# Optimization experiments

Hardware: AMD Instinct MI355X
Metric: run time of the kernel (lower is better)

## Reference

```python
import math
import jax, jax.numpy as jnp
import numpy as np

EMBED_DIM = 1024
N_HEADS = 16
HEAD_DIM = EMBED_DIM // N_HEADS
B, T = 4, 2048


def setup_inputs() -> dict:
    key = jax.random.key(0)
    k1, k2, k3 = jax.random.split(key, 3)
    scale_in = 1.0 / math.sqrt(EMBED_DIM)
    return {
        "x": jax.random.normal(k1, (B, T, EMBED_DIM), dtype=jnp.float32),
        "direction": 0,  # 0=FORWARD (causal), 1=RETRODICTION (anti-causal), 2=CORRECTION (causal)
        "qkv_w": jax.random.normal(k2, (EMBED_DIM, 3 * EMBED_DIM), dtype=jnp.float32) * scale_in,
        "qkv_b": jnp.zeros((3 * EMBED_DIM,), dtype=jnp.float32),
        "proj_w": jax.random.normal(k3, (EMBED_DIM, EMBED_DIM), dtype=jnp.float32) * scale_in,
        "proj_b": jnp.zeros((EMBED_DIM,), dtype=jnp.float32),
    }


def reference(x, direction, qkv_w, qkv_b, proj_w, proj_b):
    Bx, Tx, C = x.shape
    qkv = x @ qkv_w + qkv_b                        # [B,T,3C]
    q, k, v = jnp.split(qkv, 3, axis=-1)
    # [B,T,C] -> [B,H,T,D]
    def heads(t):
        return t.reshape(Bx, Tx, N_HEADS, HEAD_DIM).transpose(0, 2, 1, 3)
    q, k, v = heads(q), heads(k), heads(v)
    scale = 1.0 / math.sqrt(HEAD_DIM)
    attn = jnp.einsum('bhqd,bhkd->bhqk', q, k) * scale
    rows = jnp.arange(Tx)[:, None]
    cols = jnp.arange(Tx)[None, :]
    if direction == 1:  # RETRODICTION -> anti-causal (upper triangular allowed)
        mask = cols >= rows
    else:               # FORWARD / CORRECTION -> causal
        mask = cols <= rows
    attn = jnp.where(mask[None, None], attn, -jnp.inf)
    attn = jax.nn.softmax(attn, axis=-1)  # dropout p=0 -> identity
    out = jnp.einsum('bhqk,bhkd->bhqd', attn, v)   # [B,H,T,D]
    out = out.transpose(0, 2, 1, 3).reshape(Bx, Tx, C)
    return out @ proj_w + proj_b
```

## Files before the change

### kernel.cpp

```cpp
#include <hip/hip_runtime.h>
#include <math.h>

typedef __bf16 bf16_t;
typedef bf16_t bf16x8 __attribute__((ext_vector_type(8)));
typedef bf16_t bf16x4 __attribute__((ext_vector_type(4)));
typedef float  f32x4  __attribute__((ext_vector_type(4)));
typedef float  floatv4 __attribute__((ext_vector_type(4)));

#define AS1 __attribute__((address_space(1)))
#define AS3 __attribute__((address_space(3)))

static __device__ __forceinline__ void gld_lds16(const void* g, void* l) {
  __builtin_amdgcn_global_load_lds((const AS1 unsigned int*)g,
                                   (AS3 unsigned int*)l, 16, 0, 0);
}
static __device__ __forceinline__ void block_sync() {
  asm volatile("" ::: "memory");
  __builtin_amdgcn_s_barrier();
  asm volatile("" ::: "memory");
}

__global__ __launch_bounds__(256) void k_cast(const float* __restrict__ in,
                                              bf16_t* __restrict__ out, int n4) {
  int i = blockIdx.x * 256 + threadIdx.x;
  if (i >= n4) return;
  floatv4 v = ((const floatv4*)in)[i];
  bf16x4 o;
  o.x = (bf16_t)v.x; o.y = (bf16_t)v.y; o.z = (bf16_t)v.z; o.w = (bf16_t)v.w;
  ((bf16x4*)out)[i] = o;
}

__global__ __launch_bounds__(256) void k_transpose_cast(const float* __restrict__ in,
                                                        bf16_t* __restrict__ out,
                                                        int R, int Cc) {
  __shared__ float tile[32][33];
  int c0 = blockIdx.x * 32, r0 = blockIdx.y * 32;
  int tx = threadIdx.x, ty = threadIdx.y;
#pragma unroll
  for (int i = 0; i < 32; i += 8)
    tile[ty + i][tx] = in[(size_t)(r0 + ty + i) * Cc + c0 + tx];
  __syncthreads();
#pragma unroll
  for (int i = 0; i < 32; i += 8)
    out[(size_t)(c0 + ty + i) * R + r0 + tx] = (bf16_t)tile[tx][ty + i];
}


__global__ __launch_bounds__(512, 2) void k_gemm_qkv(
    const bf16_t* __restrict__ A, const bf16_t* __restrict__ Bt,
    const float* __restrict__ bias,
    bf16_t* __restrict__ qo, bf16_t* __restrict__ ko, bf16_t* __restrict__ vto) {
  const int K = 1024;
  __shared__ __align__(16) char smem[147456];
  const int m0 = blockIdx.x * 256, n0 = blockIdx.y * 128;
  const int t = threadIdx.x, lane = t & 63, wv = t >> 6;
  const int ln15 = lane & 15, lhi = lane >> 4;
  const int wr = wv >> 1, wc = wv & 1;

  f32x4 acc[4][4];
#pragma unroll
  for (int m = 0; m < 4; ++m)
#pragma unroll
    for (int n = 0; n < 4; ++n) acc[m][n] = (f32x4){0.f, 0.f, 0.f, 0.f};

  const bf16_t* aSrc = A + (size_t)(m0 + (t >> 7) * 16 + ln15) * K + ((t >> 6) & 1) * 32 + lhi * 8;
  const bf16_t* bSrc = Bt + (size_t)(n0 + (t >> 7) * 16 + ln15) * K + ((t >> 6) & 1) * 32 + lhi * 8;
  const int dstOff = t * 16;

  auto stage = [&](int k0, char* base) {
#pragma unroll
    for (int c = 0; c < 4; ++c)
      gld_lds16(aSrc + (size_t)c * 64 * K + k0, base + c * 8192 + dstOff);
#pragma unroll
    for (int c = 0; c < 2; ++c)
      gld_lds16(bSrc + (size_t)c * 64 * K + k0, base + 32768 + c * 8192 + dstOff);
  };
  auto compute = [&](const char* base) {
    const bf16_t* Ab = (const bf16_t*)base;
    const bf16_t* Bb = (const bf16_t*)(base + 32768);
#pragma unroll
    for (int kk = 0; kk < 2; ++kk) {
      bf16x8 af[4], bf[4];
#pragma unroll
      for (int m = 0; m < 4; ++m)
        af[m] = *(const bf16x8*)(Ab + ((wr * 4 + m) * 2 + kk) * 512 + lane * 8);
#pragma unroll
      for (int n = 0; n < 4; ++n)
        bf[n] = *(const bf16x8*)(Bb + ((wc * 4 + n) * 2 + kk) * 512 + lane * 8);
      __builtin_amdgcn_s_setprio(1);
#pragma unroll
      for (int m = 0; m < 4; ++m)
#pragma unroll
        for (int n = 0; n < 4; ++n)
          acc[m][n] = __builtin_amdgcn_mfma_f32_16x16x32_bf16(af[m], bf[n], acc[m][n], 0, 0, 0);
      __builtin_amdgcn_s_setprio(0);
    }
  };

  char* pc = smem;
  char* p1 = smem + 49152;
  char* p2 = smem + 98304;
  stage(0, pc);
  stage(64, p1);
#pragma unroll 1
  for (int it = 0; it < 16; ++it) {
    if (it + 2 < 16) {
      stage((it + 2) * 64, p2);
      asm volatile("s_waitcnt vmcnt(12)" ::: "memory");
    } else if (it + 1 < 16) {
      asm volatile("s_waitcnt vmcnt(6)" ::: "memory");
    } else {
      asm volatile("s_waitcnt vmcnt(0)" ::: "memory");
    }
    block_sync();
    compute(pc);
    block_sync();
    char* old = pc; pc = p1; p1 = p2; p2 = old;
  }

  const int which = n0 >> 10;
  const float bscale = (which == 0) ? 0.18033688011112042f : 1.0f;
  bf16_t* L = (bf16_t*)smem;
#pragma unroll
  for (int n = 0; n < 4; ++n) {
    const int col = wc * 64 + n * 16 + ln15;
    const float bv = bias[n0 + col];
#pragma unroll
    for (int m = 0; m < 4; ++m)
#pragma unroll
      for (int j = 0; j < 4; ++j) {
        const int row = wr * 64 + m * 16 + lhi * 4 + j;
        const bf16_t ob = (bf16_t)((acc[m][n][j] + bv) * bscale);
        if (which == 2) L[col * 264 + row] = ob;
        else            L[row * 132 + col] = ob;
      }
  }
  block_sync();
  const int bq = m0 >> 11, ttb = m0 & 2047;
  if (which == 2) {
#pragma unroll
    for (int c = 0; c < 8; ++c) {
      const int idx = c * 512 + t;
      const int vcol = idx >> 5, r8 = (idx & 31) * 8;
      bf16x8 v8 = *(const bf16x8*)&L[vcol * 264 + r8];
      const int cc = (n0 + vcol) & 1023;
      const int hh = cc >> 6, d = cc & 63;
      *(bf16x8*)&vto[((size_t)(bq * 16 + hh) * 64 + d) * 2048 + ttb + r8] = v8;
    }
  } else {
    bf16_t* dst = (which == 0) ? qo : ko;
#pragma unroll
    for (int c = 0; c < 8; ++c) {
      const int idx = c * 512 + t;
      const int row = idx >> 4, c8 = (idx & 15) * 8;
      bf16x8 v8 = *(const bf16x8*)&L[row * 132 + c8];
      const int cc = (n0 & 1023) + c8;
      const int hh = cc >> 6, d = cc & 63;
      *(bf16x8*)&dst[((size_t)(bq * 16 + hh) * 2048 + ttb + row) * 64 + d] = v8;
    }
  }
}

__global__ __launch_bounds__(256) void k_attn3(
    const bf16_t* __restrict__ q, const bf16_t* __restrict__ k,
    const bf16_t* __restrict__ vt, const int* __restrict__ dirp,
    bf16_t* __restrict__ a2) {
  const int T = 2048;
  __shared__ __align__(16) bf16_t smem[16384];
  const int bh = blockIdx.x, b = bh >> 4, h = bh & 15;
  const int jb = blockIdx.y;
  const int t = threadIdx.x, lane = t & 63, w = t >> 6;
  const int ln15 = lane & 15, lhi = lane >> 4;
  const bool anti = (*dirp == 1);

  const bf16_t* kbase = k + (size_t)bh * T * 64;
  const bf16_t* vbase = vt + (size_t)bh * 64 * T;

  auto stage = [&](int kc0, int buf) {
    char* Kd = (char*)smem + buf * 16384;
    char* Vd = Kd + 8192;
#pragma unroll
    for (int s = 0; s < 2; ++s) {
      const int qk = s * 4 + (t >> 6);
      const int krow = kc0 + (qk >> 2) * 32 + ((qk >> 1) & 1) * 4 +
                       ((lane & 15) >> 2) * 8 + (lane & 3);
      const int kcolb = (lane >> 4) * 16 + (qk & 1) * 64;
      gld_lds16((const char*)kbase + (size_t)krow * 128 + kcolb,
                Kd + s * 4096 + t * 16);
      const int gv = qk;
      const int vd = (gv & 3) * 16 + (lane & 15);
      gld_lds16((const char*)vbase + (size_t)vd * 4096 + (size_t)kc0 * 2 +
                    (gv >> 2) * 64 + (lane >> 4) * 16,
                Vd + s * 4096 + t * 16);
    }
  };

#pragma unroll 1
  for (int sel = 0; sel < 2; ++sel) {
    const int qt = sel ? (31 - jb) : jb;
    const int q0 = qt * 64 + w * 16;
    const int qrow = q0 + ln15;

    const bf16_t* qp = q + ((size_t)bh * T + qrow) * 64 + lhi * 8;
    bf16x8 qf0 = *(const bf16x8*)qp;
    bf16x8 qf1 = *(const bf16x8*)(qp + 32);

    f32x4 acc[4];
#pragma unroll
    for (int g = 0; g < 4; ++g) acc[g] = (f32x4){0.f, 0.f, 0.f, 0.f};
    float mrun = -3.0e38f, lrun = 0.f;

    const int kt0 = anti ? qt : 0;
    const int nb = anti ? (32 - qt) : (qt + 1);

    stage(kt0 * 64, 0);
#pragma unroll 1
    for (int i = 0; i < nb; ++i) {
      const int kt = kt0 + i;
      const int buf = i & 1;
      if (i + 1 < nb) {
        stage((kt + 1) * 64, buf ^ 1);
        asm volatile("s_waitcnt vmcnt(4)" ::: "memory");
      } else {
        asm volatile("s_waitcnt vmcnt(0)" ::: "memory");
      }
      block_sync();
      const bf16_t* Kb = smem + buf * 8192;
      const bf16_t* Vb = Kb + 4096;

      float sc[16];
#pragma unroll
      for (int kh = 0; kh < 2; ++kh) {
        bf16x8 k0 = *(const bf16x8*)(Kb + (kh * 4 + 0) * 512 + lane * 8);
        bf16x8 k1 = *(const bf16x8*)(Kb + (kh * 4 + 1) * 512 + lane * 8);
        bf16x8 k2 = *(const bf16x8*)(Kb + (kh * 4 + 2) * 512 + lane * 8);
        bf16x8 k3 = *(const bf16x8*)(Kb + (kh * 4 + 3) * 512 + lane * 8);
        const f32x4 zz = (f32x4){0.f, 0.f, 0.f, 0.f};
        f32x4 slo = __builtin_amdgcn_mfma_f32_16x16x32_bf16(k0, qf0, zz, 0, 0, 0);
        slo = __builtin_amdgcn_mfma_f32_16x16x32_bf16(k1, qf1, slo, 0, 0, 0);
        f32x4 shi = __builtin_amdgcn_mfma_f32_16x16x32_bf16(k2, qf0, zz, 0, 0, 0);
        shi = __builtin_amdgcn_mfma_f32_16x16x32_bf16(k3, qf1, shi, 0, 0, 0);
#pragma unroll
        for (int j = 0; j < 4; ++j) {
          sc[kh * 8 + j] = slo[j];
          sc[kh * 8 + 4 + j] = shi[j];
        }
      }
      if (kt == qt) {
#pragma unroll
        for (int e = 0; e < 16; ++e) {
          const int col = kt * 64 + (e >> 3) * 32 + lhi * 8 + (e & 7);
          const bool ok = anti ? (col >= qrow) : (col <= qrow);
          sc[e] = ok ? sc[e] : -3.0e38f;
        }
      }
      float lmax = sc[0];
#pragma unroll
      for (int e = 1; e < 16; ++e) lmax = fmaxf(lmax, sc[e]);
      if (!__all(lmax <= mrun + 8.f)) {
        float vm = lmax;
        vm = fmaxf(vm, __shfl_xor(vm, 16));
        vm = fmaxf(vm, __shfl_xor(vm, 32));
        const float mn = fmaxf(mrun, vm);
        const float al = __builtin_amdgcn_exp2f(mrun - mn);
        lrun *= al;
#pragma unroll
        for (int g = 0; g < 4; ++g) acc[g] *= al;
        mrun = mn;
      }
      bf16x8 pb0, pb1;
      float rs = 0.f;
#pragma unroll
      for (int e = 0; e < 8; ++e) {
        float p = __builtin_amdgcn_exp2f(sc[e] - mrun);
        rs += p; pb0[e] = (bf16_t)p;
      }
#pragma unroll
      for (int e = 0; e < 8; ++e) {
        float p = __builtin_amdgcn_exp2f(sc[8 + e] - mrun);
        rs += p; pb1[e] = (bf16_t)p;
      }
      lrun += rs;
#pragma unroll
      for (int dg = 0; dg < 4; ++dg) {
        bf16x8 v0 = *(const bf16x8*)(Vb + dg * 512 + lane * 8);
        acc[dg] = __builtin_amdgcn_mfma_f32_16x16x32_bf16(v0, pb0, acc[dg], 0, 0, 0);
      }
#pragma unroll
      for (int dg = 0; dg < 4; ++dg) {
        bf16x8 v1 = *(const bf16x8*)(Vb + (4 + dg) * 512 + lane * 8);
        acc[dg] = __builtin_amdgcn_mfma_f32_16x16x32_bf16(v1, pb1, acc[dg], 0, 0, 0);
      }
      block_sync();
    }

    lrun += __shfl_xor(lrun, 16);
    lrun += __shfl_xor(lrun, 32);
    const float inv = __builtin_amdgcn_rcpf(lrun);
    bf16_t* op = a2 + ((size_t)b * T + qrow) * 1024 + h * 64 + lhi * 4;
#pragma unroll
    for (int g = 0; g < 4; ++g) {
      bf16x4 o4;
#pragma unroll
      for (int jx = 0; jx < 4; ++jx) o4[jx] = (bf16_t)(acc[g][jx] * inv);
      *(bf16x4*)(op + g * 16) = o4;
    }
  }
}

__global__ __launch_bounds__(512, 2) void k_gemm_proj(
    const bf16_t* __restrict__ A, const bf16_t* __restrict__ Bt,
    const float* __restrict__ bias, float* __restrict__ out) {
  const int K = 1024;
  __shared__ __align__(16) char smem[147456];
  const int m0 = blockIdx.x * 256, n0 = blockIdx.y * 128;
  const int t = threadIdx.x, lane = t & 63, wv = t >> 6;
  const int ln15 = lane & 15, lhi = lane >> 4;
  const int wr = wv >> 1, wc = wv & 1;

  f32x4 acc[4][4];
#pragma unroll
  for (int m = 0; m < 4; ++m)
#pragma unroll
    for (int n = 0; n < 4; ++n) acc[m][n] = (f32x4){0.f, 0.f, 0.f, 0.f};

  const bf16_t* aSrc = A + (size_t)(m0 + (t >> 7) * 16 + ln15) * K + ((t >> 6) & 1) * 32 + lhi * 8;
  const bf16_t* bSrc = Bt + (size_t)(n0 + (t >> 7) * 16 + ln15) * K + ((t >> 6) & 1) * 32 + lhi * 8;
  const int dstOff = t * 16;

  auto stage = [&](int k0, char* base) {
#pragma unroll
    for (int c = 0; c < 4; ++c)
      gld_lds16(aSrc + (size_t)c * 64 * K + k0, base + c * 8192 + dstOff);
#pragma unroll
    for (int c = 0; c < 2; ++c)
      gld_lds16(bSrc + (size_t)c * 64 * K + k0, base + 32768 + c * 8192 + dstOff);
  };
  auto compute = [&](const char* base) {
    const bf16_t* Ab = (const bf16_t*)base;
    const bf16_t* Bb = (const bf16_t*)(base + 32768);
#pragma unroll
    for (int kk = 0; kk < 2; ++kk) {
      bf16x8 af[4], bf[4];
#pragma unroll
      for (int m = 0; m < 4; ++m)
        af[m] = *(const bf16x8*)(Ab + ((wr * 4 + m) * 2 + kk) * 512 + lane * 8);
#pragma unroll
      for (int n = 0; n < 4; ++n)
        bf[n] = *(const bf16x8*)(Bb + ((wc * 4 + n) * 2 + kk) * 512 + lane * 8);
      __builtin_amdgcn_s_setprio(1);
#pragma unroll
      for (int m = 0; m < 4; ++m)
#pragma unroll
        for (int n = 0; n < 4; ++n)
          acc[m][n] = __builtin_amdgcn_mfma_f32_16x16x32_bf16(af[m], bf[n], acc[m][n], 0, 0, 0);
      __builtin_amdgcn_s_setprio(0);
    }
  };

  char* pc = smem;
  char* p1 = smem + 49152;
  char* p2 = smem + 98304;
  stage(0, pc);
  stage(64, p1);
#pragma unroll 1
  for (int it = 0; it < 16; ++it) {
    if (it + 2 < 16) {
      stage((it + 2) * 64, p2);
      asm volatile("s_waitcnt vmcnt(12)" ::: "memory");
    } else if (it + 1 < 16) {
      asm volatile("s_waitcnt vmcnt(6)" ::: "memory");
    } else {
      asm volatile("s_waitcnt vmcnt(0)" ::: "memory");
    }
    block_sync();
    compute(pc);
    block_sync();
    char* old = pc; pc = p1; p1 = p2; p2 = old;
  }

#pragma unroll
  for (int n = 0; n < 4; ++n) {
    const int col = n0 + wc * 64 + n * 16 + ln15;
    const float bv = bias[col];
#pragma unroll
    for (int m = 0; m < 4; ++m)
#pragma unroll
      for (int j = 0; j < 4; ++j) {
        const int row = m0 + wr * 64 + m * 16 + lhi * 4 + j;
        out[(size_t)row * 1024 + col] = acc[m][n][j] + bv;
      }
  }
}

extern "C" void kernel_launch(void* const* d_in, const int* in_sizes, int n_in,
                              void* d_out, int out_size, void* d_ws, size_t ws_size,
                              hipStream_t stream) {
  (void)in_sizes; (void)n_in; (void)out_size; (void)ws_size;
  const float* x      = (const float*)d_in[0];
  const int*   dirp   = (const int*)d_in[1];
  const float* qkv_w  = (const float*)d_in[2];
  const float* qkv_b  = (const float*)d_in[3];
  const float* proj_w = (const float*)d_in[4];
  const float* proj_b = (const float*)d_in[5];
  float* out = (float*)d_out;

  char* ws = (char*)d_ws;
  bf16_t* xb   = (bf16_t*)(ws);
  bf16_t* wq_t = (bf16_t*)(ws + 16777216);
  bf16_t* wp_t = (bf16_t*)(ws + 23068672);
  bf16_t* qb   = (bf16_t*)(ws + 25165824);
  bf16_t* kb   = (bf16_t*)(ws + 41943040);
  bf16_t* vtb  = (bf16_t*)(ws + 58720256);
  bf16_t* a2   = xb;

  k_cast<<<8192, 256, 0, stream>>>(x, xb, 2097152);
  k_transpose_cast<<<dim3(96, 32), dim3(32, 8), 0, stream>>>(qkv_w, wq_t, 1024, 3072);
  k_transpose_cast<<<dim3(32, 32), dim3(32, 8), 0, stream>>>(proj_w, wp_t, 1024, 1024);
  k_gemm_qkv<<<dim3(32, 24), 512, 0, stream>>>(xb, wq_t, qkv_b, qb, kb, vtb);
  k_attn3<<<dim3(64, 16), 256, 0, stream>>>(qb, kb, vtb, dirp, a2);
  k_gemm_proj<<<dim3(32, 8), 512, 0, stream>>>(a2, wp_t, proj_b, out);
}
```

Measured before the change: 204.5 us.

## Enlarge QKV GEMM tile to 256x256 with interleaved LDS-load/MFMA schedule

The QKV projection GEMM now computes 256x256 output tiles per block (8x4 MFMA fragments per wave) instead of 256x128, halving the grid to 32x12. The main loop is double buffered instead of triple buffered, and each K-step is split into four phases that interleave LDS fragment reads, global-to-LDS staging and MFMA groups with explicit waits and barriers. The epilogue writes the wider tile in two halves through LDS. This aims to raise arithmetic intensity and overlap memory with compute, at the cost of more accumulator registers, many more barriers per iteration, and fewer blocks (384) to fill the CUs.

```diff
diff --git a/kernel.cpp b/kernel.cpp
--- a/kernel.cpp
+++ b/kernel.cpp
@@ -45,11 +45,291 @@
     out[(size_t)(c0 + ty + i) * R + r0 + tx] = (bf16_t)tile[tx][ty + i];
 }
 
-
 __global__ __launch_bounds__(512, 2) void k_gemm_qkv(
     const bf16_t* __restrict__ A, const bf16_t* __restrict__ Bt,
     const float* __restrict__ bias,
     bf16_t* __restrict__ qo, bf16_t* __restrict__ ko, bf16_t* __restrict__ vto) {
+  const int K = 1024;
+  __shared__ __align__(16) char smem[131072];
+  const int m0 = blockIdx.x * 256, n0 = blockIdx.y * 256;
+  const int t = threadIdx.x, lane = t & 63, wv = t >> 6;
+  const int ln15 = lane & 15, lhi = lane >> 4;
+  const int wr = wv >> 2, wc = wv & 3;
+
+  f32x4 acc[8][4];
+#pragma unroll
+  for (int m = 0; m < 8; ++m)
+#pragma unroll
+    for (int n = 0; n < 4; ++n) acc[m][n] = (f32x4){0.f, 0.f, 0.f, 0.f};
+  bf16x8 af[4], bfr[4];
+
+  auto stageA = [&](int r, int k0, char* buf) {
+    const int s = r * 8 + wv;
+    gld_lds16(A + (size_t)(m0 + (s & 15) * 16 + ln15) * K + k0 + (s >> 4) * 32 + lhi * 8,
+              buf + r * 8192 + t * 16);
+  };
+  auto stageB = [&](int r, int k0, char* buf) {
+    const int s = r * 8 + wv;
+    gld_lds16(Bt + (size_t)(n0 + (s & 15) * 16 + ln15) * K + k0 + (s >> 4) * 32 + lhi * 8,
+              buf + 32768 + r * 8192 + t * 16);
+  };
+
+#define LDA(kk, mb) do { _Pragma("unroll") for (int m = 0; m < 4; ++m) \
+    af[m] = *(const bf16x8*)((const bf16_t*)bufC + ((kk) * 16 + wr * 8 + (mb) + m) * 512 + lane * 8); } while (0)
+#define LDB(kk) do { _Pragma("unroll") for (int n = 0; n < 4; ++n) \
+    bfr[n] = *(const bf16x8*)((const bf16_t*)(bufC + 32768) + ((kk) * 16 + wc * 4 + n) * 512 + lane * 8); } while (0)
+#define MFMA16(mb) do { __builtin_amdgcn_s_setprio(1); _Pragma("unroll") \
+    for (int m = 0; m < 4; ++m) { _Pragma("unroll") for (int n = 0; n < 4; ++n) \
+      acc[(mb) + m][n] = __builtin_amdgcn_mfma_f32_16x16x32_bf16(af[m], bfr[n], acc[(mb) + m][n], 0, 0, 0); } \
+    __builtin_amdgcn_s_setprio(0); } while (0)
+#define WAIT_LGK() do { asm volatile("s_waitcnt lgkmcnt(0)" ::: "memory"); \
+    __builtin_amdgcn_sched_barrier(0); } while (0)
+
+  char* bufC = smem;
+  char* bufN = smem + 65536;
+  stageA(0, 0, bufC); stageA(1, 0, bufC); stageB(0, 0, bufC); stageB(1, 0, bufC);
+  stageA(2, 0, bufC); stageA(3, 0, bufC); stageB(2, 0, bufC); stageB(3, 0, bufC);
+  asm volatile("s_waitcnt vmcnt(4)" ::: "memory");
+  block_sync();
+
+#pragma unroll 1
+  for (int it = 0; it < 16; ++it) {
+    const int k0n = (it + 1) * 64;
+    const bool st = (it < 15);
+    LDA(0, 0); LDB(0);
+    if (st) { stageA(0, k0n, bufN); stageA(1, k0n, bufN); }
+    block_sync();
+    WAIT_LGK();
+    MFMA16(0);
+    block_sync();
+    LDA(0, 4);
+    if (st) { stageB(0, k0n, bufN); stageB(1, k0n, bufN); }
+    block_sync();
+    WAIT_LGK();
+    MFMA16(4);
+    if (st) asm volatile("s_waitcnt vmcnt(4)" ::: "memory");
+    else    asm volatile("s_waitcnt vmcnt(0)" ::: "memory");
+    block_sync();
+    LDA(1, 0); LDB(1);
+    if (st) { stageA(2, k0n, bufN); stageA(3, k0n, bufN); }
+    block_sync();
+    WAIT_LGK();
+    MFMA16(0);
+    block_sync();
+    LDA(1, 4);
+    if (st) { stageB(2, k0n, bufN); stageB(3, k0n, bufN); }
+    block_sync();
+    WAIT_LGK();
+    MFMA16(4);
+    if (st) asm volatile("s_waitcnt vmcnt(4)" ::: "memory");
+    block_sync();
+    char* tmp = bufC; bufC = bufN; bufN = tmp;
+  }
+#undef LDA
+#undef LDB
+#undef MFMA16
+#undef WAIT_LGK
+
+  const int which = n0 >> 10;
+  const float bscale = (which == 0) ? 0.18033688011112042f : 1.0f;
+  bf16_t* L = (bf16_t*)smem;
+  const int bq = m0 >> 11, ttb = m0 & 2047;
+#pragma unroll 1
+  for (int h2 = 0; h2 < 2; ++h2) {
+    if ((wc >> 1) == h2) {
+      const int colb = (wc & 1) * 64;
+#pragma unroll
+      for (int n = 0; n < 4; ++n) {
+        const int colL = colb + n * 16 + ln15;
+        const float bv = bias[n0 + h2 * 128 + colL];
+#pragma unroll
+        for (int m = 0; m < 8; ++m)
+#pragma unroll
+          for (int j = 0; j < 4; ++j) {
+            const int row = wr * 128 + m * 16 + lhi * 4 + j;
+            const bf16_t ob = (bf16_t)((acc[m][n][j] + bv) * bscale);
+            if (which == 2) L[colL * 264 + row] = ob;
+            else            L[row * 132 + colL] = ob;
+          }
+      }
+    }
+    block_sync();
+    if (which == 2) {
+#pragma unroll
+      for (int c = 0; c < 8; ++c) {
+        const int idx = c * 512 + t;
+        const int vcol = idx >> 5, r8 = (idx & 31) * 8;
+        bf16x8 v8 = *(const bf16x8*)&L[vcol * 264 + r8];
+        const int cc = (n0 + h2 * 128 + vcol) & 1023;
+        const int hh = cc >> 6, d = cc & 63;
+        *(bf16x8*)&vto[((size_t)(bq * 16 + hh) * 64 + d) * 2048 + ttb + r8] = v8;
+      }
+    } else {
+      bf16_t* dst = (which == 0) ? qo : ko;
+#pragma unroll
+      for (int c = 0; c < 8; ++c) {
+        const int idx = c * 512 + t;
+        const int row = idx >> 4, c8 = (idx & 15) * 8;
+        bf16x8 v8 = *(const bf16x8*)&L[row * 132 + c8];
+        const int cc = (n0 & 1023) + h2 * 128 + c8;
+        const int hh = cc >> 6, d = cc & 63;
+        *(bf16x8*)&dst[((size_t)(bq * 16 + hh) * 2048 + ttb + row) * 64 + d] = v8;
+      }
+    }
+    block_sync();
+  }
+}
+
+__global__ __launch_bounds__(256) void k_attn3(
+    const bf16_t* __restrict__ q, const bf16_t* __restrict__ k,
+    const bf16_t* __restrict__ vt, const int* __restrict__ dirp,
+    bf16_t* __restrict__ a2) {
+  const int T = 2048;
+  __shared__ __align__(16) bf16_t smem[16384];
+  const int bh = blockIdx.x, b = bh >> 4, h = bh & 15;
+  const int jb = blockIdx.y;
+  const int t = threadIdx.x, lane = t & 63, w = t >> 6;
+  const int ln15 = lane & 15, lhi = lane >> 4;
+  const bool anti = (*dirp == 1);
+
+  const bf16_t* kbase = k + (size_t)bh * T * 64;
+  const bf16_t* vbase = vt + (size_t)bh * 64 * T;
+
+  auto stage = [&](int kc0, int buf) {
+    char* Kd = (char*)smem + buf * 16384;
+    char* Vd = Kd + 8192;
+#pragma unroll
+    for (int s = 0; s < 2; ++s) {
+      const int qk = s * 4 + (t >> 6);
+      const int krow = kc0 + (qk >> 2) * 32 + ((qk >> 1) & 1) * 4 +
+                       ((lane & 15) >> 2) * 8 + (lane & 3);
+      const int kcolb = (lane >> 4) * 16 + (qk & 1) * 64;
+      gld_lds16((const char*)kbase + (size_t)krow * 128 + kcolb,
+                Kd + s * 4096 + t * 16);
+      const int gv = qk;
+      const int vd = (gv & 3) * 16 + (lane & 15);
+      gld_lds16((const char*)vbase + (size_t)vd * 4096 + (size_t)kc0 * 2 +
+                    (gv >> 2) * 64 + (lane >> 4) * 16,
+                Vd + s * 4096 + t * 16);
+    }
+  };
+
+#pragma unroll 1
+  for (int sel = 0; sel < 2; ++sel) {
+    const int qt = sel ? (31 - jb) : jb;
+    const int q0 = qt * 64 + w * 16;
+    const int qrow = q0 + ln15;
+
+    const bf16_t* qp = q + ((size_t)bh * T + qrow) * 64 + lhi * 8;
+    bf16x8 qf0 = *(const bf16x8*)qp;
+    bf16x8 qf1 = *(const bf16x8*)(qp + 32);
+
+    f32x4 acc[4];
+#pragma unroll
+    for (int g = 0; g < 4; ++g) acc[g] = (f32x4){0.f, 0.f, 0.f, 0.f};
+    float mrun = -3.0e38f, lrun = 0.f;
+
+    const int kt0 = anti ? qt : 0;
+    const int nb = anti ? (32 - qt) : (qt + 1);
+
+    stage(kt0 * 64, 0);
+#pragma unroll 1
+    for (int i = 0; i < nb; ++i) {
+      const int kt = kt0 + i;
+      const int buf = i & 1;
+      if (i + 1 < nb) {
+        stage((kt + 1) * 64, buf ^ 1);
+        asm volatile("s_waitcnt vmcnt(4)" ::: "memory");
+      } else {
+        asm volatile("s_waitcnt vmcnt(0)" ::: "memory");
+      }
+      block_sync();
+      const bf16_t* Kb = smem + buf * 8192;
+      const bf16_t* Vb = Kb + 4096;
+
+      float sc[16];
+#pragma unroll
+      for (int kh = 0; kh < 2; ++kh) {
+        bf16x8 k0 = *(const bf16x8*)(Kb + (kh * 4 + 0) * 512 + lane * 8);
+        bf16x8 k1 = *(const bf16x8*)(Kb + (kh * 4 + 1) * 512 + lane * 8);
+        bf16x8 k2 = *(const bf16x8*)(Kb + (kh * 4 + 2) * 512 + lane * 8);
+        bf16x8 k3 = *(const bf16x8*)(Kb + (kh * 4 + 3) * 512 + lane * 8);
+        const f32x4 zz = (f32x4){0.f, 0.f, 0.f, 0.f};
+        f32x4 slo = __builtin_amdgcn_mfma_f32_16x16x32_bf16(k0, qf0, zz, 0, 0, 0);
+        slo = __builtin_amdgcn_mfma_f32_16x16x32_bf16(k1, qf1, slo, 0, 0, 0);
+        f32x4 shi = __builtin_amdgcn_mfma_f32_16x16x32_bf16(k2, qf0, zz, 0, 0, 0);
+        shi = __builtin_amdgcn_mfma_f32_16x16x32_bf16(k3, qf1, shi, 0, 0, 0);
+#pragma unroll
+        for (int j = 0; j < 4; ++j) {
+          sc[kh * 8 + j] = slo[j];
+          sc[kh * 8 + 4 + j] = shi[j];
+        }
+      }
+      if (kt == qt) {
+#pragma unroll
+        for (int e = 0; e < 16; ++e) {
+          const int col = kt * 64 + (e >> 3) * 32 + lhi * 8 + (e & 7);
+          const bool ok = anti ? (col >= qrow) : (col <= qrow);
+          sc[e] = ok ? sc[e] : -3.0e38f;
+        }
+      }
+      float lmax = sc[0];
+#pragma unroll
+      for (int e = 1; e < 16; ++e) lmax = fmaxf(lmax, sc[e]);
+      if (!__all(lmax <= mrun + 8.f)) {
+        float vm = lmax;
+        vm = fmaxf(vm, __shfl_xor(vm, 16));
+        vm = fmaxf(vm, __shfl_xor(vm, 32));
+        const float mn = fmaxf(mrun, vm);
+        const float al = __builtin_amdgcn_exp2f(mrun - mn);
+        lrun *= al;
+#pragma unroll
+        for (int g = 0; g < 4; ++g) acc[g] *= al;
+        mrun = mn;
+      }
+      bf16x8 pb0, pb1;
+      float rs = 0.f;
+#pragma unroll
+      for (int e = 0; e < 8; ++e) {
+        float p = __builtin_amdgcn_exp2f(sc[e] - mrun);
+        rs += p; pb0[e] = (bf16_t)p;
+      }
+#pragma unroll
+      for (int e = 0; e < 8; ++e) {
+        float p = __builtin_amdgcn_exp2f(sc[8 + e] - mrun);
+        rs += p; pb1[e] = (bf16_t)p;
+      }
+      lrun += rs;
+#pragma unroll
+      for (int dg = 0; dg < 4; ++dg) {
+        bf16x8 v0 = *(const bf16x8*)(Vb + dg * 512 + lane * 8);
+        acc[dg] = __builtin_amdgcn_mfma_f32_16x16x32_bf16(v0, pb0, acc[dg], 0, 0, 0);
+      }
+#pragma unroll
+      for (int dg = 0; dg < 4; ++dg) {
+        bf16x8 v1 = *(const bf16x8*)(Vb + (4 + dg) * 512 + lane * 8);
+        acc[dg] = __builtin_amdgcn_mfma_f32_16x16x32_bf16(v1, pb1, acc[dg], 0, 0, 0);
+      }
+      block_sync();
+    }
+
+    lrun += __shfl_xor(lrun, 16);
+    lrun += __shfl_xor(lrun, 32);
+    const float inv = __builtin_amdgcn_rcpf(lrun);
+    bf16_t* op = a2 + ((size_t)b * T + qrow) * 1024 + h * 64 + lhi * 4;
+#pragma unroll
+    for (int g = 0; g < 4; ++g) {
+      bf16x4 o4;
+#pragma unroll
+      for (int jx = 0; jx < 4; ++jx) o4[jx] = (bf16_t)(acc[g][jx] * inv);
+      *(bf16x4*)(op + g * 16) = o4;
+    }
+  }
+}
+
+__global__ __launch_bounds__(512, 2) void k_gemm_proj(
+    const bf16_t* __restrict__ A, const bf16_t* __restrict__ Bt,
+    const float* __restrict__ bias, float* __restrict__ out) {
   const int K = 1024;
   __shared__ __align__(16) char smem[147456];
   const int m0 = blockIdx.x * 256, n0 = blockIdx.y * 128;
@@ -118,267 +398,6 @@
     char* old = pc; pc = p1; p1 = p2; p2 = old;
   }
 
-  const int which = n0 >> 10;
-  const float bscale = (which == 0) ? 0.18033688011112042f : 1.0f;
-  bf16_t* L = (bf16_t*)smem;
-#pragma unroll
-  for (int n = 0; n < 4; ++n) {
-    const int col = wc * 64 + n * 16 + ln15;
-    const float bv = bias[n0 + col];
-#pragma unroll
-    for (int m = 0; m < 4; ++m)
-#pragma unroll
-      for (int j = 0; j < 4; ++j) {
-        const int row = wr * 64 + m * 16 + lhi * 4 + j;
-        const bf16_t ob = (bf16_t)((acc[m][n][j] + bv) * bscale);
-        if (which == 2) L[col * 264 + row] = ob;
-        else            L[row * 132 + col] = ob;
-      }
-  }
-  block_sync();
-  const int bq = m0 >> 11, ttb = m0 & 2047;
-  if (which == 2) {
-#pragma unroll
-    for (int c = 0; c < 8; ++c) {
-      const int idx = c * 512 + t;
-      const int vcol = idx >> 5, r8 = (idx & 31) * 8;
-      bf16x8 v8 = *(const bf16x8*)&L[vcol * 264 + r8];
-      const int cc = (n0 + vcol) & 1023;
-      const int hh = cc >> 6, d = cc & 63;
-      *(bf16x8*)&vto[((size_t)(bq * 16 + hh) * 64 + d) * 2048 + ttb + r8] = v8;
-    }
-  } else {
-    bf16_t* dst = (which == 0) ? qo : ko;
-#pragma unroll
-    for (int c = 0; c < 8; ++c) {
-      const int idx = c * 512 + t;
-      const int row = idx >> 4, c8 = (idx & 15) * 8;
-      bf16x8 v8 = *(const bf16x8*)&L[row * 132 + c8];
-      const int cc = (n0 & 1023) + c8;
-      const int hh = cc >> 6, d = cc & 63;
-      *(bf16x8*)&dst[((size_t)(bq * 16 + hh) * 2048 + ttb + row) * 64 + d] = v8;
-    }
-  }
-}
-
-__global__ __launch_bounds__(256) void k_attn3(
-    const bf16_t* __restrict__ q, const bf16_t* __restrict__ k,
-    const bf16_t* __restrict__ vt, const int* __restrict__ dirp,
-    bf16_t* __restrict__ a2) {
-  const int T = 2048;
-  __shared__ __align__(16) bf16_t smem[16384];
-  const int bh = blockIdx.x, b = bh >> 4, h = bh & 15;
-  const int jb = blockIdx.y;
-  const int t = threadIdx.x, lane = t & 63, w = t >> 6;
-  const int ln15 = lane & 15, lhi = lane >> 4;
-  const bool anti = (*dirp == 1);
-
-  const bf16_t* kbase = k + (size_t)bh * T * 64;
-  const bf16_t* vbase = vt + (size_t)bh * 64 * T;
-
-  auto stage = [&](int kc0, int buf) {
-    char* Kd = (char*)smem + buf * 16384;
-    char* Vd = Kd + 8192;
-#pragma unroll
-    for (int s = 0; s < 2; ++s) {
-      const int qk = s * 4 + (t >> 6);
-      const int krow = kc0 + (qk >> 2) * 32 + ((qk >> 1) & 1) * 4 +
-                       ((lane & 15) >> 2) * 8 + (lane & 3);
-      const int kcolb = (lane >> 4) * 16 + (qk & 1) * 64;
-      gld_lds16((const char*)kbase + (size_t)krow * 128 + kcolb,
-                Kd + s * 4096 + t * 16);
-      const int gv = qk;
-      const int vd = (gv & 3) * 16 + (lane & 15);
-      gld_lds16((const char*)vbase + (size_t)vd * 4096 + (size_t)kc0 * 2 +
-                    (gv >> 2) * 64 + (lane >> 4) * 16,
-                Vd + s * 4096 + t * 16);
-    }
-  };
-
-#pragma unroll 1
-  for (int sel = 0; sel < 2; ++sel) {
-    const int qt = sel ? (31 - jb) : jb;
-    const int q0 = qt * 64 + w * 16;
-    const int qrow = q0 + ln15;
-
-    const bf16_t* qp = q + ((size_t)bh * T + qrow) * 64 + lhi * 8;
-    bf16x8 qf0 = *(const bf16x8*)qp;
-    bf16x8 qf1 = *(const bf16x8*)(qp + 32);
-
-    f32x4 acc[4];
-#pragma unroll
-    for (int g = 0; g < 4; ++g) acc[g] = (f32x4){0.f, 0.f, 0.f, 0.f};
-    float mrun = -3.0e38f, lrun = 0.f;
-
-    const int kt0 = anti ? qt : 0;
-    const int nb = anti ? (32 - qt) : (qt + 1);
-
-    stage(kt0 * 64, 0);
-#pragma unroll 1
-    for (int i = 0; i < nb; ++i) {
-      const int kt = kt0 + i;
-      const int buf = i & 1;
-      if (i + 1 < nb) {
-        stage((kt + 1) * 64, buf ^ 1);
-        asm volatile("s_waitcnt vmcnt(4)" ::: "memory");
-      } else {
-        asm volatile("s_waitcnt vmcnt(0)" ::: "memory");
-      }
-      block_sync();
-      const bf16_t* Kb = smem + buf * 8192;
-      const bf16_t* Vb = Kb + 4096;
-
-      float sc[16];
-#pragma unroll
-      for (int kh = 0; kh < 2; ++kh) {
-        bf16x8 k0 = *(const bf16x8*)(Kb + (kh * 4 + 0) * 512 + lane * 8);
-        bf16x8 k1 = *(const bf16x8*)(Kb + (kh * 4 + 1) * 512 + lane * 8);
-        bf16x8 k2 = *(const bf16x8*)(Kb + (kh * 4 + 2) * 512 + lane * 8);
-        bf16x8 k3 = *(const bf16x8*)(Kb + (kh * 4 + 3) * 512 + lane * 8);
-        const f32x4 zz = (f32x4){0.f, 0.f, 0.f, 0.f};
-        f32x4 slo = __builtin_amdgcn_mfma_f32_16x16x32_bf16(k0, qf0, zz, 0, 0, 0);
-        slo = __builtin_amdgcn_mfma_f32_16x16x32_bf16(k1, qf1, slo, 0, 0, 0);
-        f32x4 shi = __builtin_amdgcn_mfma_f32_16x16x32_bf16(k2, qf0, zz, 0, 0, 0);
-        shi = __builtin_amdgcn_mfma_f32_16x16x32_bf16(k3, qf1, shi, 0, 0, 0);
-#pragma unroll
-        for (int j = 0; j < 4; ++j) {
-          sc[kh * 8 + j] = slo[j];
-          sc[kh * 8 + 4 + j] = shi[j];
-        }
-      }
-      if (kt == qt) {
-#pragma unroll
-        for (int e = 0; e < 16; ++e) {
-          const int col = kt * 64 + (e >> 3) * 32 + lhi * 8 + (e & 7);
-          const bool ok = anti ? (col >= qrow) : (col <= qrow);
-          sc[e] = ok ? sc[e] : -3.0e38f;
-        }
-      }
-      float lmax = sc[0];
-#pragma unroll
-      for (int e = 1; e < 16; ++e) lmax = fmaxf(lmax, sc[e]);
-      if (!__all(lmax <= mrun + 8.f)) {
-        float vm = lmax;
-        vm = fmaxf(vm, __shfl_xor(vm, 16));
-        vm = fmaxf(vm, __shfl_xor(vm, 32));
-        const float mn = fmaxf(mrun, vm);
-        const float al = __builtin_amdgcn_exp2f(mrun - mn);
-        lrun *= al;
-#pragma unroll
-        for (int g = 0; g < 4; ++g) acc[g] *= al;
-        mrun = mn;
-      }
-      bf16x8 pb0, pb1;
-      float rs = 0.f;
-#pragma unroll
-      for (int e = 0; e < 8; ++e) {
-        float p = __builtin_amdgcn_exp2f(sc[e] - mrun);
-        rs += p; pb0[e] = (bf16_t)p;
-      }
-#pragma unroll
-      for (int e = 0; e < 8; ++e) {
-        float p = __builtin_amdgcn_exp2f(sc[8 + e] - mrun);
-        rs += p; pb1[e] = (bf16_t)p;
-      }
-      lrun += rs;
-#pragma unroll
-      for (int dg = 0; dg < 4; ++dg) {
-        bf16x8 v0 = *(const bf16x8*)(Vb + dg * 512 + lane * 8);
-        acc[dg] = __builtin_amdgcn_mfma_f32_16x16x32_bf16(v0, pb0, acc[dg], 0, 0, 0);
-      }
-#pragma unroll
-      for (int dg = 0; dg < 4; ++dg) {
-        bf16x8 v1 = *(const bf16x8*)(Vb + (4 + dg) * 512 + lane * 8);
-        acc[dg] = __builtin_amdgcn_mfma_f32_16x16x32_bf16(v1, pb1, acc[dg], 0, 0, 0);
-      }
-      block_sync();
-    }
-
-    lrun += __shfl_xor(lrun, 16);
-    lrun += __shfl_xor(lrun, 32);
-    const float inv = __builtin_amdgcn_rcpf(lrun);
-    bf16_t* op = a2 + ((size_t)b * T + qrow) * 1024 + h * 64 + lhi * 4;
-#pragma unroll
-    for (int g = 0; g < 4; ++g) {
-      bf16x4 o4;
-#pragma unroll
-      for (int jx = 0; jx < 4; ++jx) o4[jx] = (bf16_t)(acc[g][jx] * inv);
-      *(bf16x4*)(op + g * 16) = o4;
-    }
-  }
-}
-
-__global__ __launch_bounds__(512, 2) void k_gemm_proj(
-    const bf16_t* __restrict__ A, const bf16_t* __restrict__ Bt,
-    const float* __restrict__ bias, float* __restrict__ out) {
-  const int K = 1024;
-  __shared__ __align__(16) char smem[147456];
-  const int m0 = blockIdx.x * 256, n0 = blockIdx.y * 128;
-  const int t = threadIdx.x, lane = t & 63, wv = t >> 6;
-  const int ln15 = lane & 15, lhi = lane >> 4;
-  const int wr = wv >> 1, wc = wv & 1;
-
-  f32x4 acc[4][4];
-#pragma unroll
-  for (int m = 0; m < 4; ++m)
-#pragma unroll
-    for (int n = 0; n < 4; ++n) acc[m][n] = (f32x4){0.f, 0.f, 0.f, 0.f};
-
-  const bf16_t* aSrc = A + (size_t)(m0 + (t >> 7) * 16 + ln15) * K + ((t >> 6) & 1) * 32 + lhi * 8;
-  const bf16_t* bSrc = Bt + (size_t)(n0 + (t >> 7) * 16 + ln15) * K + ((t >> 6) & 1) * 32 + lhi * 8;
-  const int dstOff = t * 16;
-
-  auto stage = [&](int k0, char* base) {
-#pragma unroll
-    for (int c = 0; c < 4; ++c)
-      gld_lds16(aSrc + (size_t)c * 64 * K + k0, base + c * 8192 + dstOff);
-#pragma unroll
-    for (int c = 0; c < 2; ++c)
-      gld_lds16(bSrc + (size_t)c * 64 * K + k0, base + 32768 + c * 8192 + dstOff);
-  };
-  auto compute = [&](const char* base) {
-    const bf16_t* Ab = (const bf16_t*)base;
-    const bf16_t* Bb = (const bf16_t*)(base + 32768);
-#pragma unroll
-    for (int kk = 0; kk < 2; ++kk) {
-      bf16x8 af[4], bf[4];
-#pragma unroll
-      for (int m = 0; m < 4; ++m)
-        af[m] = *(const bf16x8*)(Ab + ((wr * 4 + m) * 2 + kk) * 512 + lane * 8);
-#pragma unroll
-      for (int n = 0; n < 4; ++n)
-        bf[n] = *(const bf16x8*)(Bb + ((wc * 4 + n) * 2 + kk) * 512 + lane * 8);
-      __builtin_amdgcn_s_setprio(1);
-#pragma unroll
-      for (int m = 0; m < 4; ++m)
-#pragma unroll
-        for (int n = 0; n < 4; ++n)
-          acc[m][n] = __builtin_amdgcn_mfma_f32_16x16x32_bf16(af[m], bf[n], acc[m][n], 0, 0, 0);
-      __builtin_amdgcn_s_setprio(0);
-    }
-  };
-
-  char* pc = smem;
-  char* p1 = smem + 49152;
-  char* p2 = smem + 98304;
-  stage(0, pc);
-  stage(64, p1);
-#pragma unroll 1
-  for (int it = 0; it < 16; ++it) {
-    if (it + 2 < 16) {
-      stage((it + 2) * 64, p2);
-      asm volatile("s_waitcnt vmcnt(12)" ::: "memory");
-    } else if (it + 1 < 16) {
-      asm volatile("s_waitcnt vmcnt(6)" ::: "memory");
-    } else {
-      asm volatile("s_waitcnt vmcnt(0)" ::: "memory");
-    }
-    block_sync();
-    compute(pc);
-    block_sync();
-    char* old = pc; pc = p1; p1 = p2; p2 = old;
-  }
-
 #pragma unroll
   for (int n = 0; n < 4; ++n) {
     const int col = n0 + wc * 64 + n * 16 + ln15;
@@ -417,7 +436,7 @@
   k_cast<<<8192, 256, 0, stream>>>(x, xb, 2097152);
   k_transpose_cast<<<dim3(96, 32), dim3(32, 8), 0, stream>>>(qkv_w, wq_t, 1024, 3072);
   k_transpose_cast<<<dim3(32, 32), dim3(32, 8), 0, stream>>>(proj_w, wp_t, 1024, 1024);
-  k_gemm_qkv<<<dim3(32, 24), 512, 0, stream>>>(xb, wq_t, qkv_b, qb, kb, vtb);
+  k_gemm_qkv<<<dim3(32, 12), 512, 0, stream>>>(xb, wq_t, qkv_b, qb, kb, vtb);
   k_attn3<<<dim3(64, 16), 256, 0, stream>>>(qb, kb, vtb, dirp, a2);
   k_gemm_proj<<<dim3(32, 8), 512, 0, stream>>>(a2, wp_t, proj_b, out);
 }
```

Result: no change. 206.5 us (+1.0%).
